# Performance work log

Hardware: AMD Instinct MI355X
Metric: run time of the kernel (lower is better)

## Reference

```python
import jax, jax.numpy as jnp
import numpy as np
from jax import lax

S, B, H, V = 512, 256, 512, 256


def setup_inputs() -> dict:
    key = jax.random.key(0)
    ks = jax.random.split(key, 8)
    enc_outs = jax.random.normal(ks[0], (S, B, H), dtype=jnp.float32)
    # projection Linear(hidden -> vocab)
    W = jax.random.normal(ks[1], (H, V), dtype=jnp.float32) * (1.0 / np.sqrt(H))
    b = jnp.zeros((V,), dtype=jnp.float32)
    # xavier_normal_ for transition: std = sqrt(2/(V+V))
    transition = jax.random.normal(ks[2], (V, V), dtype=jnp.float32) * np.sqrt(2.0 / (V + V))
    start_transition = jax.random.normal(ks[3], (V,), dtype=jnp.float32)
    end_transition = jax.random.normal(ks[4], (V,), dtype=jnp.float32)
    targets = jax.random.randint(ks[5], (S, B), 0, V, dtype=jnp.int32)
    lengths = jax.random.randint(ks[6], (B,), 1, S + 1, dtype=jnp.int32)
    return {"enc_outs": enc_outs, "W": W, "b": b, "transition": transition,
            "start_transition": start_transition, "end_transition": end_transition,
            "targets": targets, "lengths": lengths}


def reference(enc_outs, W, b, transition, start_transition, end_transition, targets, lengths):
    # forward(): Linear + log_softmax -> logits (S, B, V)
    logits = jax.nn.log_softmax(enc_outs @ W + b, axis=-1)
    # make_length_mask then transpose -> (S, B)
    mask = (jnp.arange(S)[:, None] < lengths[None, :]).astype(logits.dtype)

    # ---- partition (forward algorithm) ----
    Z0 = start_transition[None, :] + logits[0]  # (B, V)

    def step(Z, xs):
        logit_t, m_t = xs  # (B, V), (B,)
        # Z_new[b, j] = logsumexp_i(Z[b, i] + trans[i, j]) + emit[b, j]
        Zn = jax.scipy.special.logsumexp(Z[:, :, None] + transition[None, :, :], axis=1) + logit_t
        m = m_t[:, None]
        return Zn * m + Z * (1.0 - m), None

    Zf, _ = lax.scan(step, Z0, (logits[1:], mask[1:]))
    Zp = jax.scipy.special.logsumexp(Zf + end_transition[None, :], axis=-1)  # (B,)

    # ---- score of gold path ----
    curr, nxt = targets[:-1], targets[1:]  # (S-1, B)
    trans_sc = transition[curr, nxt]       # (S-1, B)
    emit_sc = jnp.take_along_axis(logits[:-1], curr[:, :, None], axis=2)[..., 0]  # (S-1, B)
    score = start_transition[targets[0]] + jnp.sum(trans_sc * mask[1:] + emit_sc * mask[:-1], axis=0)
    last_idx = (jnp.sum(mask, axis=0) - 1.0).astype(jnp.int32)  # (B,)
    last_target = targets[last_idx, jnp.arange(B)]              # (B,)
    last_emit = jnp.take_along_axis(logits[-1], last_target[:, None], axis=1)[:, 0]
    score = score + end_transition[last_target] + last_emit * mask[-1]

    # ---- loss ----
    return jnp.mean(Zp - score)
```

## Files before the change

kernel.cpp:

```cpp
#include <hip/hip_runtime.h>

#define S_LEN 512
#define BATCH 256
#define HID   512
#define VOC   256

typedef __attribute__((ext_vector_type(8))) short short8;
typedef __attribute__((ext_vector_type(4))) float f32x4;
typedef __attribute__((ext_vector_type(2))) _Float16 h2;

static __device__ __forceinline__ unsigned short f2bf(float f){
  unsigned int u = __builtin_bit_cast(unsigned int, f);
  u += 0x7fffu + ((u >> 16) & 1u);
  return (unsigned short)(u >> 16);
}
static __device__ __forceinline__ unsigned short f2h(float f){
  _Float16 h = (_Float16)f;
  return __builtin_bit_cast(unsigned short, h);
}
static __device__ __forceinline__ float h2f(unsigned short u){
  return (float)__builtin_bit_cast(_Float16, u);
}
static __device__ __forceinline__ float dot2(h2 a, h2 b, float c){
#if __has_builtin(__builtin_amdgcn_fdot2)
  return __builtin_amdgcn_fdot2(a, b, c, false);
#else
  return c + (float)a[0]*(float)b[0] + (float)a[1]*(float)b[1];
#endif
}

__global__ void prep_kernel(const float* __restrict__ trans, const float* __restrict__ W,
                            unsigned short* __restrict__ expTt, unsigned short* __restrict__ Wt){
  int idx = blockIdx.x * 256 + threadIdx.x;
  if (idx < VOC*VOC){
    int j = idx >> 8, i = idx & 255;
    expTt[idx] = f2h(__expf(trans[i*VOC + j]));
  } else {
    int k2 = idx - VOC*VOC;
    if (k2 < VOC*HID){
      int n = k2 >> 9, k = k2 & 511;
      Wt[k2] = f2bf(W[k*VOC + n]);
    }
  }
}

#define LDA 40
__global__ __launch_bounds__(256) void gemm_ls_kernel(
    const float* __restrict__ enc, const unsigned short* __restrict__ Wt,
    const float* __restrict__ bias, unsigned short* __restrict__ logits)
{
  __shared__ __align__(16) unsigned short Als[64*LDA];
  __shared__ __align__(16) unsigned short Bls[256*LDA];
  __shared__ float bls[256];

  int tid  = threadIdx.x;
  int lane = tid & 63, wv = tid >> 6;
  int l15  = lane & 15, g4 = lane >> 4;
  int r = tid >> 2, c = (tid & 3) * 8;
  int rowBlock = blockIdx.x * 64;

  if (tid < 256) bls[tid] = bias[tid];

  f32x4 acc[16];
  #pragma unroll
  for (int j=0;j<16;j++) acc[j] = (f32x4){0.f,0.f,0.f,0.f};

  for (int k0 = 0; k0 < HID; k0 += 32){
    __syncthreads();
    const float* ap = enc + (rowBlock + r)*HID + k0 + c;
    float4 a0 = *(const float4*)ap;
    float4 a1 = *(const float4*)(ap + 4);
    short8 av;
    av[0]=(short)f2bf(a0.x); av[1]=(short)f2bf(a0.y); av[2]=(short)f2bf(a0.z); av[3]=(short)f2bf(a0.w);
    av[4]=(short)f2bf(a1.x); av[5]=(short)f2bf(a1.y); av[6]=(short)f2bf(a1.z); av[7]=(short)f2bf(a1.w);
    *(short8*)&Als[r*LDA + c] = av;
    const uint4* bp = (const uint4*)(Wt + tid*HID + k0);
    uint4 b0 = bp[0], b1 = bp[1], b2 = bp[2], b3 = bp[3];
    uint4* bd = (uint4*)&Bls[tid*LDA];
    bd[0]=b0; bd[1]=b1; bd[2]=b2; bd[3]=b3;
    __syncthreads();
    short8 afr = *(const short8*)&Als[(wv*16 + l15)*LDA + g4*8];
    #pragma unroll
    for (int j=0;j<16;j++){
      short8 bfr = *(const short8*)&Bls[(j*16 + l15)*LDA + g4*8];
      acc[j] = __builtin_amdgcn_mfma_f32_16x16x32_bf16(afr, bfr, acc[j], 0, 0, 0);
    }
  }

  #pragma unroll
  for (int reg=0; reg<4; ++reg){
    float x[16];
    float m = -1e30f;
    #pragma unroll
    for (int j=0;j<16;j++){ x[j] = acc[j][reg] + bls[j*16 + l15]; m = fmaxf(m, x[j]); }
    #pragma unroll
    for (int msk=1; msk<16; msk<<=1) m = fmaxf(m, __shfl_xor(m, msk));
    float s = 0.f;
    #pragma unroll
    for (int j=0;j<16;j++) s += __expf(x[j] - m);
    #pragma unroll
    for (int msk=1; msk<16; msk<<=1) s += __shfl_xor(s, msk);
    float lse = m + __logf(s);
    int row = rowBlock + wv*16 + g4*4 + reg;
    unsigned short* op = logits + row*VOC + l15;
    #pragma unroll
    for (int j=0;j<16;j++) op[j*16] = f2h(x[j] - lse);
  }
}

__global__ __launch_bounds__(512) void scan_kernel(
    const unsigned short* __restrict__ logits,
    const unsigned short* __restrict__ expTt,
    const float* __restrict__ trans,
    const float* __restrict__ startT,
    const float* __restrict__ endT,
    const int* __restrict__ targets,
    const int* __restrict__ lengths,
    float* __restrict__ out)
{
  int b   = blockIdx.x;
  int tid = threadIdx.x;
  int j   = tid & 255;
  int g   = tid >> 8;
  int len = lengths[b];

  __shared__ __align__(16) float Zs[256];
  __shared__ __align__(16) float ph[2][256];
  __shared__ __align__(16) unsigned short e16[256];
  __shared__ float wmax[4];
  __shared__ float red[16];

  h2 wreg[64];
  {
    const uint4* cp = (const uint4*)(expTt + j*VOC + g*128);
    #pragma unroll
    for (int p=0;p<16;p++){
      uint4 q = cp[p];
      wreg[4*p+0] = __builtin_bit_cast(h2, q.x);
      wreg[4*p+1] = __builtin_bit_cast(h2, q.y);
      wreg[4*p+2] = __builtin_bit_cast(h2, q.z);
      wreg[4*p+3] = __builtin_bit_cast(h2, q.w);
    }
  }

  if (tid < 256){
    float z = startT[j] + h2f(logits[b*VOC + j]);
    Zs[j] = z;
    float m = z;
    #pragma unroll
    for (int msk=1; msk<64; msk<<=1) m = fmaxf(m, __shfl_xor(m, msk));
    if ((tid & 63) == 0) wmax[tid >> 6] = m;
  }
  __syncthreads();

  float mcur = 0.f, lg = 0.f;
  for (int t = 1; t < len; ++t){
    if (tid < 256){
      lg   = h2f(logits[(t*BATCH + b)*VOC + j]);
      mcur = fmaxf(fmaxf(wmax[0], wmax[1]), fmaxf(wmax[2], wmax[3]));
      e16[j] = f2h(__expf(Zs[j] - mcur));
    }
    __syncthreads();
    {
      float acc0 = 0.f, acc1 = 0.f;
      const uint4* ep = (const uint4*)(e16 + g*128);
      #pragma unroll
      for (int p=0;p<16;p++){
        uint4 q = ep[p];
        acc0 = dot2(__builtin_bit_cast(h2, q.x), wreg[4*p+0], acc0);
        acc1 = dot2(__builtin_bit_cast(h2, q.y), wreg[4*p+1], acc1);
        acc0 = dot2(__builtin_bit_cast(h2, q.z), wreg[4*p+2], acc0);
        acc1 = dot2(__builtin_bit_cast(h2, q.w), wreg[4*p+3], acc1);
      }
      ph[g][j] = acc0 + acc1;
    }
    __syncthreads();
    if (tid < 256){
      float zn = mcur + __logf(ph[0][j] + ph[1][j]) + lg;
      Zs[j] = zn;
      float m = zn;
      #pragma unroll
      for (int msk=1; msk<64; msk<<=1) m = fmaxf(m, __shfl_xor(m, msk));
      if ((tid & 63) == 0) wmax[tid >> 6] = m;
    }
    __syncthreads();
  }

  float v = 0.f;
  if (tid < 256){
    v = Zs[j] + endT[j];
    float m = v;
    #pragma unroll
    for (int msk=1; msk<64; msk<<=1) m = fmaxf(m, __shfl_xor(m, msk));
    if ((tid & 63) == 0) red[tid >> 6] = m;
  }
  __syncthreads();
  float m3 = fmaxf(fmaxf(red[0], red[1]), fmaxf(red[2], red[3]));
  if (tid < 256){
    float e = __expf(v - m3);
    #pragma unroll
    for (int msk=1; msk<64; msk<<=1) e += __shfl_xor(e, msk);
    if ((tid & 63) == 0) red[4 + (tid >> 6)] = e;
  }
  float sc = 0.f;
  {
    int t = tid;
    if (t < len){
      int tg = targets[t*BATCH + b];
      sc = h2f(logits[(t*BATCH + b)*VOC + tg]);
      if (t >= 1){
        int tp = targets[(t-1)*BATCH + b];
        sc += trans[tp*VOC + tg];
      } else {
        sc += startT[tg];
      }
      if (t == len - 1) sc += endT[tg];
    }
    #pragma unroll
    for (int msk=1; msk<64; msk<<=1) sc += __shfl_xor(sc, msk);
    if ((tid & 63) == 0) red[8 + (tid >> 6)] = sc;
  }
  __syncthreads();
  if (tid == 0){
    float s3 = red[4] + red[5] + red[6] + red[7];
    float Zp = m3 + __logf(s3);
    float score = red[8]+red[9]+red[10]+red[11]+red[12]+red[13]+red[14]+red[15];
    atomicAdd(out, (Zp - score) * (1.0f / BATCH));
  }
}

extern "C" void kernel_launch(void* const* d_in, const int* in_sizes, int n_in,
                              void* d_out, int out_size, void* d_ws, size_t ws_size,
                              hipStream_t stream){
  const float* enc    = (const float*)d_in[0];
  const float* W      = (const float*)d_in[1];
  const float* bias   = (const float*)d_in[2];
  const float* trans  = (const float*)d_in[3];
  const float* startT = (const float*)d_in[4];
  const float* endT   = (const float*)d_in[5];
  const int*   targets= (const int*)d_in[6];
  const int*   lengths= (const int*)d_in[7];

  unsigned short* logits = (unsigned short*)d_ws;
  unsigned short* expTt  = logits + (size_t)S_LEN*BATCH*VOC;
  unsigned short* Wt     = expTt + (size_t)VOC*VOC;

  hipMemsetAsync(d_out, 0, sizeof(float)*out_size, stream);
  prep_kernel<<<(VOC*VOC + VOC*HID)/256, 256, 0, stream>>>(trans, W, expTt, Wt);
  gemm_ls_kernel<<<(S_LEN*BATCH)/64, 256, 0, stream>>>(enc, Wt, bias, logits);
  scan_kernel<<<BATCH, 512, 0, stream>>>(logits, expTt, trans, startT, endT, targets, lengths, (float*)d_out);
}
```

Measured before the change: 958.3 us.

## Run CRF forward recursion in probability space with retiled GEMM and single-barrier scan

The GEMM is retiled to 128-row blocks with 512 threads and a 4x4 MFMA tile per wave. It now writes normalized softmax probabilities in fp16 rather than log-probabilities. The scan runs the forward algorithm in linear space with per-step renormalization accumulated as a log constant. Each thread owns a full column of exp(transition) in registers, so there is one barrier per step instead of three, plus double-buffered LDS and prefetch of the next step's emissions. This cuts the serial per-step latency and the exp/log work, but fp16 probabilities can underflow, and the gold-path score now takes the log of clamped probabilities.

```diff
diff --git a/kernel.cpp b/kernel.cpp
--- a/kernel.cpp
+++ b/kernel.cpp
@@ -27,6 +27,16 @@
 #else
   return c + (float)a[0]*(float)b[0] + (float)a[1]*(float)b[1];
 #endif
+}
+static __device__ __forceinline__ float wave_sum(float v){
+  #pragma unroll
+  for (int m = 1; m < 64; m <<= 1) v += __shfl_xor(v, m);
+  return v;
+}
+static __device__ __forceinline__ void sync_lds(){
+  asm volatile("s_waitcnt lgkmcnt(0)" ::: "memory");
+  __builtin_amdgcn_s_barrier();
+  asm volatile("" ::: "memory");
 }
 
 __global__ void prep_kernel(const float* __restrict__ trans, const float* __restrict__ W,
@@ -44,72 +54,128 @@
   }
 }
 
-#define LDA 40
-__global__ __launch_bounds__(256) void gemm_ls_kernel(
+#define BM  128
+#define BK  64
+#define LDT 72
+
+__global__ __launch_bounds__(512, 4) void gemm_ls_kernel(
     const float* __restrict__ enc, const unsigned short* __restrict__ Wt,
-    const float* __restrict__ bias, unsigned short* __restrict__ logits)
+    const float* __restrict__ bias, unsigned short* __restrict__ probs)
 {
-  __shared__ __align__(16) unsigned short Als[64*LDA];
-  __shared__ __align__(16) unsigned short Bls[256*LDA];
-  __shared__ float bls[256];
-
-  int tid  = threadIdx.x;
-  int lane = tid & 63, wv = tid >> 6;
-  int l15  = lane & 15, g4 = lane >> 4;
-  int r = tid >> 2, c = (tid & 3) * 8;
-  int rowBlock = blockIdx.x * 64;
-
-  if (tid < 256) bls[tid] = bias[tid];
-
-  f32x4 acc[16];
-  #pragma unroll
-  for (int j=0;j<16;j++) acc[j] = (f32x4){0.f,0.f,0.f,0.f};
-
-  for (int k0 = 0; k0 < HID; k0 += 32){
+  __shared__ __align__(16) unsigned short Als[BM * LDT];
+  __shared__ __align__(16) unsigned short Bls[VOC * LDT];
+  __shared__ float pmax[4][BM];
+  __shared__ float psum[4][BM];
+
+  const int tid  = threadIdx.x;
+  const int lane = tid & 63, w = tid >> 6;
+  const int l15  = lane & 15, g4 = lane >> 4;
+  const int wm   = w >> 2, wn = w & 3;
+  const int row0 = blockIdx.x * BM;
+
+  const int ar = tid >> 2, ac = (tid & 3) * 16;
+  const int bn = tid >> 1, bk = (tid & 1) * 32;
+
+  f32x4 acc[4][4];
+  #pragma unroll
+  for (int i = 0; i < 4; i++)
+    #pragma unroll
+    for (int j = 0; j < 4; j++) acc[i][j] = (f32x4){0.f,0.f,0.f,0.f};
+
+  const float* aBase = enc + (size_t)(row0 + ar) * HID + ac;
+  const unsigned short* bBase = Wt + (size_t)bn * HID + bk;
+
+  for (int k0 = 0; k0 < HID; k0 += BK){
     __syncthreads();
-    const float* ap = enc + (rowBlock + r)*HID + k0 + c;
-    float4 a0 = *(const float4*)ap;
-    float4 a1 = *(const float4*)(ap + 4);
-    short8 av;
-    av[0]=(short)f2bf(a0.x); av[1]=(short)f2bf(a0.y); av[2]=(short)f2bf(a0.z); av[3]=(short)f2bf(a0.w);
-    av[4]=(short)f2bf(a1.x); av[5]=(short)f2bf(a1.y); av[6]=(short)f2bf(a1.z); av[7]=(short)f2bf(a1.w);
-    *(short8*)&Als[r*LDA + c] = av;
-    const uint4* bp = (const uint4*)(Wt + tid*HID + k0);
-    uint4 b0 = bp[0], b1 = bp[1], b2 = bp[2], b3 = bp[3];
-    uint4* bd = (uint4*)&Bls[tid*LDA];
-    bd[0]=b0; bd[1]=b1; bd[2]=b2; bd[3]=b3;
+    const float4* ap = (const float4*)(aBase + k0);
+    float4 a0 = ap[0], a1 = ap[1], a2 = ap[2], a3 = ap[3];
+    short8 s0, s1;
+    s0[0]=(short)f2bf(a0.x); s0[1]=(short)f2bf(a0.y); s0[2]=(short)f2bf(a0.z); s0[3]=(short)f2bf(a0.w);
+    s0[4]=(short)f2bf(a1.x); s0[5]=(short)f2bf(a1.y); s0[6]=(short)f2bf(a1.z); s0[7]=(short)f2bf(a1.w);
+    s1[0]=(short)f2bf(a2.x); s1[1]=(short)f2bf(a2.y); s1[2]=(short)f2bf(a2.z); s1[3]=(short)f2bf(a2.w);
+    s1[4]=(short)f2bf(a3.x); s1[5]=(short)f2bf(a3.y); s1[6]=(short)f2bf(a3.z); s1[7]=(short)f2bf(a3.w);
+    *(short8*)&Als[ar*LDT + ac]     = s0;
+    *(short8*)&Als[ar*LDT + ac + 8] = s1;
+    const uint4* bp = (const uint4*)(bBase + k0);
+    uint4 q0 = bp[0], q1 = bp[1], q2 = bp[2], q3 = bp[3];
+    uint4* bd = (uint4*)&Bls[bn*LDT + bk];
+    bd[0]=q0; bd[1]=q1; bd[2]=q2; bd[3]=q3;
     __syncthreads();
-    short8 afr = *(const short8*)&Als[(wv*16 + l15)*LDA + g4*8];
-    #pragma unroll
-    for (int j=0;j<16;j++){
-      short8 bfr = *(const short8*)&Bls[(j*16 + l15)*LDA + g4*8];
-      acc[j] = __builtin_amdgcn_mfma_f32_16x16x32_bf16(afr, bfr, acc[j], 0, 0, 0);
-    }
-  }
-
-  #pragma unroll
-  for (int reg=0; reg<4; ++reg){
-    float x[16];
-    float m = -1e30f;
-    #pragma unroll
-    for (int j=0;j<16;j++){ x[j] = acc[j][reg] + bls[j*16 + l15]; m = fmaxf(m, x[j]); }
-    #pragma unroll
-    for (int msk=1; msk<16; msk<<=1) m = fmaxf(m, __shfl_xor(m, msk));
-    float s = 0.f;
-    #pragma unroll
-    for (int j=0;j<16;j++) s += __expf(x[j] - m);
-    #pragma unroll
-    for (int msk=1; msk<16; msk<<=1) s += __shfl_xor(s, msk);
-    float lse = m + __logf(s);
-    int row = rowBlock + wv*16 + g4*4 + reg;
-    unsigned short* op = logits + row*VOC + l15;
-    #pragma unroll
-    for (int j=0;j<16;j++) op[j*16] = f2h(x[j] - lse);
-  }
-}
-
-__global__ __launch_bounds__(512) void scan_kernel(
-    const unsigned short* __restrict__ logits,
+    #pragma unroll
+    for (int s = 0; s < 2; s++){
+      short8 af[4];
+      #pragma unroll
+      for (int mi = 0; mi < 4; mi++)
+        af[mi] = *(const short8*)&Als[(wm*64 + mi*16 + l15)*LDT + s*32 + g4*8];
+      #pragma unroll
+      for (int ni = 0; ni < 4; ni++){
+        short8 bf = *(const short8*)&Bls[(wn*64 + ni*16 + l15)*LDT + s*32 + g4*8];
+        #pragma unroll
+        for (int mi = 0; mi < 4; mi++)
+          acc[mi][ni] = __builtin_amdgcn_mfma_f32_16x16x32_bf16(af[mi], bf, acc[mi][ni], 0, 0, 0);
+      }
+    }
+  }
+
+  float bcol[4];
+  #pragma unroll
+  for (int ni = 0; ni < 4; ni++) bcol[ni] = bias[wn*64 + ni*16 + l15];
+
+  #pragma unroll
+  for (int mi = 0; mi < 4; mi++){
+    #pragma unroll
+    for (int r = 0; r < 4; r++){
+      float m = acc[mi][0][r] + bcol[0];
+      #pragma unroll
+      for (int ni = 1; ni < 4; ni++) m = fmaxf(m, acc[mi][ni][r] + bcol[ni]);
+      #pragma unroll
+      for (int msk = 1; msk < 16; msk <<= 1) m = fmaxf(m, __shfl_xor(m, msk));
+      if (l15 == 0) pmax[wn][wm*64 + mi*16 + g4*4 + r] = m;
+    }
+  }
+  __syncthreads();
+  float rowm[4][4];
+  #pragma unroll
+  for (int mi = 0; mi < 4; mi++)
+    #pragma unroll
+    for (int r = 0; r < 4; r++){
+      int rl = wm*64 + mi*16 + g4*4 + r;
+      rowm[mi][r] = fmaxf(fmaxf(pmax[0][rl], pmax[1][rl]), fmaxf(pmax[2][rl], pmax[3][rl]));
+    }
+  #pragma unroll
+  for (int mi = 0; mi < 4; mi++){
+    #pragma unroll
+    for (int r = 0; r < 4; r++){
+      float sum = 0.f;
+      #pragma unroll
+      for (int ni = 0; ni < 4; ni++){
+        float e = __expf(acc[mi][ni][r] + bcol[ni] - rowm[mi][r]);
+        acc[mi][ni][r] = e;
+        sum += e;
+      }
+      #pragma unroll
+      for (int msk = 1; msk < 16; msk <<= 1) sum += __shfl_xor(sum, msk);
+      if (l15 == 0) psum[wn][wm*64 + mi*16 + g4*4 + r] = sum;
+    }
+  }
+  __syncthreads();
+  #pragma unroll
+  for (int mi = 0; mi < 4; mi++){
+    #pragma unroll
+    for (int r = 0; r < 4; r++){
+      int rl = wm*64 + mi*16 + g4*4 + r;
+      float sv = (psum[0][rl] + psum[1][rl]) + (psum[2][rl] + psum[3][rl]);
+      float invs = __builtin_amdgcn_rcpf(sv);
+      size_t base = (size_t)(row0 + rl) * VOC + wn*64 + l15;
+      #pragma unroll
+      for (int ni = 0; ni < 4; ni++)
+        probs[base + ni*16] = f2h(acc[mi][ni][r] * invs);
+    }
+  }
+}
+
+__global__ __launch_bounds__(256) void scan_kernel(
+    const unsigned short* __restrict__ probs,
     const unsigned short* __restrict__ expTt,
     const float* __restrict__ trans,
     const float* __restrict__ startT,
@@ -118,23 +184,19 @@
     const int* __restrict__ lengths,
     float* __restrict__ out)
 {
-  int b   = blockIdx.x;
-  int tid = threadIdx.x;
-  int j   = tid & 255;
-  int g   = tid >> 8;
-  int len = lengths[b];
-
-  __shared__ __align__(16) float Zs[256];
-  __shared__ __align__(16) float ph[2][256];
-  __shared__ __align__(16) unsigned short e16[256];
-  __shared__ float wmax[4];
-  __shared__ float red[16];
-
-  h2 wreg[64];
-  {
-    const uint4* cp = (const uint4*)(expTt + j*VOC + g*128);
-    #pragma unroll
-    for (int p=0;p<16;p++){
+  const int b = blockIdx.x;
+  const int j = threadIdx.x;
+  const int len = lengths[b];
+
+  __shared__ __align__(16) unsigned short ubuf[2][VOC];
+  __shared__ __align__(16) float pb[2][4];
+  __shared__ float red[8];
+
+  h2 wreg[128];
+  {
+    const uint4* cp = (const uint4*)(expTt + (size_t)j * VOC);
+    #pragma unroll
+    for (int p = 0; p < 32; p++){
       uint4 q = cp[p];
       wreg[4*p+0] = __builtin_bit_cast(h2, q.x);
       wreg[4*p+1] = __builtin_bit_cast(h2, q.y);
@@ -143,88 +205,70 @@
     }
   }
 
-  if (tid < 256){
-    float z = startT[j] + h2f(logits[b*VOC + j]);
-    Zs[j] = z;
-    float m = z;
-    #pragma unroll
-    for (int msk=1; msk<64; msk<<=1) m = fmaxf(m, __shfl_xor(m, msk));
-    if ((tid & 63) == 0) wmax[tid >> 6] = m;
-  }
-  __syncthreads();
-
-  float mcur = 0.f, lg = 0.f;
+  float aval = __expf(startT[j]) * h2f(probs[b*VOC + j]);
+  ubuf[0][j] = f2h(aval);
+  {
+    float ws = wave_sum(aval);
+    if ((j & 63) == 0) pb[0][j >> 6] = ws;
+  }
+  unsigned short pnext = probs[((size_t)BATCH + b) * VOC + j];
+  float C = 0.f;
+  sync_lds();
+
   for (int t = 1; t < len; ++t){
-    if (tid < 256){
-      lg   = h2f(logits[(t*BATCH + b)*VOC + j]);
-      mcur = fmaxf(fmaxf(wmax[0], wmax[1]), fmaxf(wmax[2], wmax[3]));
-      e16[j] = f2h(__expf(Zs[j] - mcur));
-    }
-    __syncthreads();
-    {
-      float acc0 = 0.f, acc1 = 0.f;
-      const uint4* ep = (const uint4*)(e16 + g*128);
-      #pragma unroll
-      for (int p=0;p<16;p++){
-        uint4 q = ep[p];
-        acc0 = dot2(__builtin_bit_cast(h2, q.x), wreg[4*p+0], acc0);
-        acc1 = dot2(__builtin_bit_cast(h2, q.y), wreg[4*p+1], acc1);
-        acc0 = dot2(__builtin_bit_cast(h2, q.z), wreg[4*p+2], acc0);
-        acc1 = dot2(__builtin_bit_cast(h2, q.w), wreg[4*p+3], acc1);
-      }
-      ph[g][j] = acc0 + acc1;
-    }
-    __syncthreads();
-    if (tid < 256){
-      float zn = mcur + __logf(ph[0][j] + ph[1][j]) + lg;
-      Zs[j] = zn;
-      float m = zn;
-      #pragma unroll
-      for (int msk=1; msk<64; msk<<=1) m = fmaxf(m, __shfl_xor(m, msk));
-      if ((tid & 63) == 0) wmax[tid >> 6] = m;
-    }
-    __syncthreads();
-  }
-
-  float v = 0.f;
-  if (tid < 256){
-    v = Zs[j] + endT[j];
-    float m = v;
-    #pragma unroll
-    for (int msk=1; msk<64; msk<<=1) m = fmaxf(m, __shfl_xor(m, msk));
-    if ((tid & 63) == 0) red[tid >> 6] = m;
-  }
-  __syncthreads();
-  float m3 = fmaxf(fmaxf(red[0], red[1]), fmaxf(red[2], red[3]));
-  if (tid < 256){
-    float e = __expf(v - m3);
-    #pragma unroll
-    for (int msk=1; msk<64; msk<<=1) e += __shfl_xor(e, msk);
-    if ((tid & 63) == 0) red[4 + (tid >> 6)] = e;
+    const int cur = t & 1, prv = cur ^ 1;
+    float4 pp = *(const float4*)&pb[prv][0];
+    float s = (pp.x + pp.y) + (pp.z + pp.w);
+    float inv = __builtin_amdgcn_rcpf(s);
+    C += __logf(s);
+    float pcur = h2f(pnext);
+    int tn = (t + 1 < S_LEN) ? (t + 1) : (S_LEN - 1);
+    pnext = probs[((size_t)tn * BATCH + b) * VOC + j];
+    const uint4* up = (const uint4*)&ubuf[prv][0];
+    float a0 = 0.f, a1 = 0.f, a2 = 0.f, a3 = 0.f;
+    #pragma unroll
+    for (int q = 0; q < 32; q++){
+      uint4 v = up[q];
+      a0 = dot2(__builtin_bit_cast(h2, v.x), wreg[4*q+0], a0);
+      a1 = dot2(__builtin_bit_cast(h2, v.y), wreg[4*q+1], a1);
+      a2 = dot2(__builtin_bit_cast(h2, v.z), wreg[4*q+2], a2);
+      a3 = dot2(__builtin_bit_cast(h2, v.w), wreg[4*q+3], a3);
+    }
+    float qd = (a0 + a1) + (a2 + a3);
+    aval = qd * inv * pcur;
+    ubuf[cur][j] = f2h(aval);
+    float ws = wave_sum(aval);
+    if ((j & 63) == 0) pb[cur][j >> 6] = ws;
+    sync_lds();
+  }
+
+  {
+    float v = aval * __expf(endT[j]);
+    float ws = wave_sum(v);
+    if ((j & 63) == 0) red[j >> 6] = ws;
   }
   float sc = 0.f;
-  {
-    int t = tid;
+  #pragma unroll
+  for (int half = 0; half < 2; ++half){
+    int t = j + half * 256;
     if (t < len){
       int tg = targets[t*BATCH + b];
-      sc = h2f(logits[(t*BATCH + b)*VOC + tg]);
-      if (t >= 1){
-        int tp = targets[(t-1)*BATCH + b];
-        sc += trans[tp*VOC + tg];
-      } else {
-        sc += startT[tg];
-      }
+      float p = h2f(probs[((size_t)t * BATCH + b) * VOC + tg]);
+      sc += __logf(fmaxf(p, 1e-12f));
+      if (t >= 1) sc += trans[targets[(t-1)*BATCH + b]*VOC + tg];
+      else        sc += startT[tg];
       if (t == len - 1) sc += endT[tg];
     }
-    #pragma unroll
-    for (int msk=1; msk<64; msk<<=1) sc += __shfl_xor(sc, msk);
-    if ((tid & 63) == 0) red[8 + (tid >> 6)] = sc;
-  }
-  __syncthreads();
-  if (tid == 0){
-    float s3 = red[4] + red[5] + red[6] + red[7];
-    float Zp = m3 + __logf(s3);
-    float score = red[8]+red[9]+red[10]+red[11]+red[12]+red[13]+red[14]+red[15];
+  }
+  {
+    float ws = wave_sum(sc);
+    if ((j & 63) == 0) red[4 + (j >> 6)] = ws;
+  }
+  sync_lds();
+  if (j == 0){
+    float tot = (red[0] + red[1]) + (red[2] + red[3]);
+    float Zp = C + __logf(tot);
+    float score = (red[4] + red[5]) + (red[6] + red[7]);
     atomicAdd(out, (Zp - score) * (1.0f / BATCH));
   }
 }
@@ -241,12 +285,12 @@
   const int*   targets= (const int*)d_in[6];
   const int*   lengths= (const int*)d_in[7];
 
-  unsigned short* logits = (unsigned short*)d_ws;
-  unsigned short* expTt  = logits + (size_t)S_LEN*BATCH*VOC;
-  unsigned short* Wt     = expTt + (size_t)VOC*VOC;
+  unsigned short* probs = (unsigned short*)d_ws;
+  unsigned short* expTt = probs + (size_t)S_LEN*BATCH*VOC;
+  unsigned short* Wt    = expTt + (size_t)VOC*VOC;
 
   hipMemsetAsync(d_out, 0, sizeof(float)*out_size, stream);
   prep_kernel<<<(VOC*VOC + VOC*HID)/256, 256, 0, stream>>>(trans, W, expTt, Wt);
-  gemm_ls_kernel<<<(S_LEN*BATCH)/64, 256, 0, stream>>>(enc, Wt, bias, logits);
-  scan_kernel<<<BATCH, 512, 0, stream>>>(logits, expTt, trans, startT, endT, targets, lengths, (float*)d_out);
-}
+  gemm_ls_kernel<<<(S_LEN*BATCH)/BM, 512, 0, stream>>>(enc, Wt, bias, probs);
+  scan_kernel<<<BATCH, 256, 0, stream>>>(probs, expTt, trans, startT, endT, targets, lengths, (float*)d_out);
+}
```

Measured after the change: 872.5 us. 1.1x faster.
